# Performance work log

Hardware: AMD Instinct MI355X
Metric: run time of the kernel (lower is better)

Reference implementation:

```python
import jax, jax.numpy as jnp
import numpy as np
import math

G_GRAPHS = 32   # graphs per batch
NPG = 2048      # nodes per graph
DEG = 8         # avg degree
IN_DIM = 128
HID = 128

def _lin(k, fi, fo):
    return jax.random.normal(k, (fi, fo), jnp.float32) / np.sqrt(fi).astype(np.float32)

def setup_inputs():
    key = jax.random.key(0)
    ks = jax.random.split(key, 32)
    Nt = G_GRAPHS * NPG
    Epg = NPG * DEG
    E = G_GRAPHS * Epg
    x = jax.random.normal(ks[0], (Nt, IN_DIM), jnp.float32)
    src = jax.random.randint(ks[1], (E,), 0, NPG)
    dst = jax.random.randint(ks[2], (E,), 0, NPG)
    off = (jnp.arange(E) // Epg) * NPG  # keep edges within their graph block
    edge_index = jnp.stack([src + off, dst + off]).astype(jnp.int32)
    batch = (jnp.arange(Nt) // NPG).astype(jnp.int32)
    p = {}
    dims = [(IN_DIM, HID), (HID, HID), (HID, HID), (HID, HID)]
    for i, (fi, fo) in enumerate(dims, 1):
        p['Wl%d' % i] = _lin(ks[3 * i], fi, fo)
        p['bl%d' % i] = jnp.zeros((fo,), jnp.float32)
        p['Wr%d' % i] = _lin(ks[3 * i + 1], fi, fo)
    for j in (1, 2):  # SAGPooling score GNN (GraphConv hidden->1)
        p['Prel%d' % j] = _lin(ks[15 + 2 * j], HID, 1)
        p['prb%d' % j] = jnp.zeros((1,), jnp.float32)
        p['Proot%d' % j] = _lin(ks[16 + 2 * j], HID, 1)
    p['W5'] = _lin(ks[24], HID, 64); p['b5'] = jnp.zeros((64,), jnp.float32)
    p['W6'] = _lin(ks[25], 64, 2);  p['b6'] = jnp.zeros((2,), jnp.float32)
    return dict(x=x, edge_index=edge_index, batch=batch, npg=NPG, **p)

def reference(x, edge_index, batch, npg,
              Wl1, bl1, Wr1, Wl2, bl2, Wr2, Wl3, bl3, Wr3, Wl4, bl4, Wr4,
              Prel1, prb1, Proot1, Prel2, prb2, Proot2, W5, b5, W6, b6):
    src, dst = edge_index[0], edge_index[1]
    Nt = x.shape[0]
    Gn = Nt // npg

    def sage(h, em, Wl, bl, Wr):
        # SAGEConv (mean aggr): lin_l(mean_j x_j) + lin_r(x_root)
        s = jax.ops.segment_sum(h[src] * em[:, None], dst, num_segments=Nt)
        c = jax.ops.segment_sum(em, dst, num_segments=Nt)
        return (s / jnp.maximum(c, 1.0)[:, None]) @ Wl + bl + h @ Wr

    def pool(h, em, nm, k, Prel, prb, Proot):
        # SAGPooling: score = GraphConv(h) (add aggr), top-k per graph, x *= tanh(score)
        s = jax.ops.segment_sum(h[src] * em[:, None], dst, num_segments=Nt)
        score = (s @ Prel + h @ Proot + prb)[:, 0]
        smr = jnp.where(nm > 0, score, -1e30).reshape(Gn, npg)
        _, idx = jax.lax.top_k(smr, k)
        newm = jnp.zeros((Gn, npg), h.dtype).at[jnp.arange(Gn)[:, None], idx].set(1.0).reshape(-1)
        h = h * jnp.tanh(score)[:, None] * newm[:, None]
        em = em * newm[src] * newm[dst]  # filter_adj: keep edges with both ends kept
        return h, em, newm

    em = jnp.ones(src.shape, x.dtype)
    nm = jnp.ones((Nt,), x.dtype)
    h = jax.nn.relu(sage(x, em, Wl1, bl1, Wr1))
    h = jax.nn.relu(sage(h, em, Wl2, bl2, Wr2))
    k1 = math.ceil(0.5 * npg)
    h, em, nm = pool(h, em, nm, k1, Prel1, prb1, Proot1)
    h = jax.nn.relu(sage(h, em, Wl3, bl3, Wr3)) * nm[:, None]
    h = jax.nn.relu(sage(h, em, Wl4, bl4, Wr4)) * nm[:, None]
    k2 = math.ceil(0.5 * k1)
    h, em, nm = pool(h, em, nm, k2, Prel2, prb2, Proot2)
    # global mean pool over surviving nodes
    sums = jax.ops.segment_sum(h, batch, num_segments=Gn)
    cnt = jax.ops.segment_sum(nm, batch, num_segments=Gn)
    g = sums / jnp.maximum(cnt, 1.0)[:, None]
    g = jax.nn.relu(g @ W5 + b5)
    return jax.nn.log_softmax(g @ W6 + b6, axis=1)
```

## Files before the change

kernel.cpp:

```cpp
#include <hip/hip_runtime.h>
#include <hip/hip_bf16.h>
#include <math.h>

#define NT   65536
#define NPGC 2048
#define NG   32
#define NE   524288
#define HID  128
#define K1   1024
#define K2   512

typedef short short8 __attribute__((ext_vector_type(8)));
typedef float f32x4  __attribute__((ext_vector_type(4)));

__device__ __forceinline__ float bf2f(unsigned short u) {
    union { unsigned int i; float f; } v; v.i = ((unsigned int)u) << 16; return v.f;
}
__device__ __forceinline__ unsigned short f2bf(float f) {
    union { float f; unsigned int i; } v; v.f = f;
    unsigned int x = v.i;
    return (unsigned short)((x + 0x7fffu + ((x >> 16) & 1u)) >> 16);
}
__device__ __forceinline__ void split2(float v, unsigned short& hi, unsigned short& lo) {
    unsigned int b = __float_as_uint(v);
    hi = (unsigned short)(b >> 16);
    float rem = v - __uint_as_float(b & 0xFFFF0000u);
    lo = (unsigned short)(__float_as_uint(rem) >> 16);
}

__global__ void k_detect(const unsigned short* __restrict__ x, int* __restrict__ flag) {
    __shared__ int cnt;
    if (threadIdx.x == 0) cnt = 0;
    __syncthreads();
    int sane = 0;
#pragma unroll
    for (int j = 0; j < 16; ++j) {
        unsigned short u = x[threadIdx.x * 16 + j];
        int e = (u >> 7) & 0xFF;
        if (e > 0x60 && e < 0xA0) sane++;
    }
    atomicAdd(&cnt, sane);
    __syncthreads();
    if (threadIdx.x == 0) *flag = (cnt > 3686) ? 1 : 0;
}

struct CvtDesc { const void* src[22]; int n[22]; int off[22]; };

__global__ void k_cvt(CvtDesc d, float* __restrict__ wts, const int* __restrict__ flag) {
    int t = blockIdx.y;
    int n = d.n[t];
    bool isbf = (*flag != 0);
    const unsigned short* sb = (const unsigned short*)d.src[t];
    const float* sf = (const float*)d.src[t];
    float* o = wts + d.off[t];
    for (int i = blockIdx.x * blockDim.x + threadIdx.x; i < n; i += gridDim.x * blockDim.x)
        o[i] = isbf ? bf2f(sb[i]) : sf[i];
}

__global__ void k_packW(const float* __restrict__ wts, int4 oWl, int4 oWr,
                        unsigned short* __restrict__ Wpack,
                        int* __restrict__ rowc, int* __restrict__ fill) {
    int idx = blockIdx.x * 256 + threadIdx.x;
    if (idx < NT) { rowc[idx] = 0; fill[idx] = 0; }
    if (idx >= 4 * 8 * 8 * 64 * 8) return;
    int L    = idx >> 15;
    int rem  = idx & 32767;
    int ct   = rem >> 12;
    int rem2 = rem & 4095;
    int ks   = rem2 >> 9;
    int rem3 = rem2 & 511;
    int lane = rem3 >> 3;
    int j    = rem3 & 7;
    int k   = ks * 32 + (lane >> 4) * 8 + j;
    int col = ct * 16 + (lane & 15);
    int ol = (L == 0) ? oWl.x : (L == 1) ? oWl.y : (L == 2) ? oWl.z : oWl.w;
    int orr = (L == 0) ? oWr.x : (L == 1) ? oWr.y : (L == 2) ? oWr.z : oWr.w;
    float w = (k < 128) ? wts[ol + k * 128 + col] : wts[orr + (k - 128) * 128 + col];
    unsigned short hi = f2bf(w);
    unsigned short lo = f2bf(w - bf2f(hi));
    int base = L * 65536 + (ct * 8 + ks) * 512 + lane * 8 + j;
    Wpack[base]         = hi;
    Wpack[base + 32768] = lo;
}

__global__ void k_hist(const int* __restrict__ dstE, int* __restrict__ rowc) {
    int e = blockIdx.x * 256 + threadIdx.x;
    if (e < NE) atomicAdd(&rowc[dstE[e]], 1);
}

__global__ void k_scan1(const int* __restrict__ cnt, int* __restrict__ rp, int* __restrict__ bsum,
                        float* __restrict__ invc) {
    __shared__ int s[256];
    int t = threadIdx.x;
    int i = blockIdx.x * 256 + t;
    int v = cnt[i];
    invc[i] = 1.0f / fmaxf((float)v, 1.0f);
    s[t] = v;
    __syncthreads();
    for (int off = 1; off < 256; off <<= 1) {
        int a = (t >= off) ? s[t - off] : 0;
        __syncthreads();
        s[t] += a;
        __syncthreads();
    }
    rp[i] = s[t] - v;
    if (t == 255) bsum[blockIdx.x] = s[255];
}

__global__ void k_scan23(int* __restrict__ rp, const int* __restrict__ bsum) {
    __shared__ int s[256];
    int t = threadIdx.x;
    s[t] = bsum[t];
    __syncthreads();
    for (int off = 1; off < 256; off <<= 1) {
        int a = (t >= off) ? s[t - off] : 0;
        __syncthreads();
        s[t] += a;
        __syncthreads();
    }
    int boffv = s[blockIdx.x] - bsum[blockIdx.x];
    int i = blockIdx.x * 256 + t;
    rp[i] += boffv;
    if (i == 0) rp[NT] = NE;
}

__global__ void k_scatter(const int* __restrict__ src, const int* __restrict__ dst,
                          const int* __restrict__ rp, int* __restrict__ fill, int* __restrict__ col) {
    int e = blockIdx.x * blockDim.x + threadIdx.x;
    if (e < NE) {
        int d = dst[e];
        int p = rp[d] + atomicAdd(&fill[d], 1);
        col[p] = src[e];
    }
}

__device__ __forceinline__ int lds_sw(int node, int k) {
    int g = k >> 3;
    int go = g ^ (node & 7);
    return node * 128 + go * 8 + (k & 7);
}

template<int MODE>
__device__ __forceinline__ float4 ldrow4(const void* __restrict__ h, int node, int f) {
    if constexpr (MODE == 1) {
        ushort4 v = *((const ushort4*)h + (size_t)node * 32 + (f >> 2));
        float4 o; o.x = bf2f(v.x); o.y = bf2f(v.y); o.z = bf2f(v.z); o.w = bf2f(v.w);
        return o;
    } else {
        return *((const float4*)h + (size_t)node * 32 + (f >> 2));
    }
}

template<bool HAS_TS, bool COMPACT, int MODE>
__device__ __forceinline__ void sage_body(
    const void* __restrict__ h, const float* __restrict__ ts,
    const float* __restrict__ invc,
    const int* __restrict__ rp, const int* __restrict__ col,
    const unsigned short* __restrict__ Wp,
    unsigned short* Ahi, unsigned short* Alo,
    unsigned short* Bhi, unsigned short* Blo,
    int n0, const int* __restrict__ actb, int tid, f32x4 acc[2][2])
{
    int lane = tid & 63, w = tid >> 6;
    int lrow = lane & 15, quad = lane >> 4;
    int gnode = tid >> 5;
    int f = (tid & 31) * 4;

    int gns[4], begs[4], ends[4]; float invs[4];
#pragma unroll
    for (int p = 0; p < 4; ++p) gns[p] = COMPACT ? actb[p * 8 + gnode] : n0 + p * 8 + gnode;
#pragma unroll
    for (int p = 0; p < 4; ++p) { begs[p] = rp[gns[p]]; ends[p] = rp[gns[p] + 1]; }
#pragma unroll
    for (int p = 0; p < 4; ++p) invs[p] = invc[gns[p]];

    float4 rootv[4]; float roots[4];
#pragma unroll
    for (int i = 0; i < 4; ++i) {
        int idx = i * 256 + tid;
        int node = idx >> 5;
        int f2 = (idx & 31) * 4;
        int gn = COMPACT ? actb[node] : n0 + node;
        rootv[i] = ldrow4<MODE>(h, gn, f2);
        roots[i] = HAS_TS ? ts[gn] : 1.0f;
    }

#pragma unroll
    for (int pass = 0; pass < 4; ++pass) {
        int node = pass * 8 + gnode;
        float ax = 0.f, ay = 0.f, az = 0.f, aw = 0.f;
        int beg = begs[pass], end = ends[pass];
        int ecl = end - 1;
        for (int e0 = beg; e0 < end; e0 += 8) {
            int sj[8];
#pragma unroll
            for (int j = 0; j < 8; ++j) {
                int e = (e0 + j < end) ? e0 + j : ecl;
                sj[j] = col[e];
            }
            float4 vj[8];
#pragma unroll
            for (int j = 0; j < 8; ++j)
                vj[j] = ldrow4<MODE>(h, sj[j], f);
#pragma unroll
            for (int j = 0; j < 8; ++j) {
                float cj = (e0 + j < end) ? (HAS_TS ? ts[sj[j]] : 1.0f) : 0.0f;
                ax += vj[j].x * cj;
                ay += vj[j].y * cj;
                az += vj[j].z * cj;
                aw += vj[j].w * cj;
            }
        }
        float inv = invs[pass];
        ushort4 hi4, lo4;
        split2(ax * inv, hi4.x, lo4.x);
        split2(ay * inv, hi4.y, lo4.y);
        split2(az * inv, hi4.z, lo4.z);
        split2(aw * inv, hi4.w, lo4.w);
        int a = lds_sw(node, f);
        *(ushort4*)&Ahi[a] = hi4;
        *(ushort4*)&Alo[a] = lo4;
    }

#pragma unroll
    for (int i = 0; i < 4; ++i) {
        int idx = i * 256 + tid;
        int node = idx >> 5;
        int f2 = (idx & 31) * 4;
        float sc = roots[i];
        ushort4 hi4, lo4;
        split2(rootv[i].x * sc, hi4.x, lo4.x);
        split2(rootv[i].y * sc, hi4.y, lo4.y);
        split2(rootv[i].z * sc, hi4.z, lo4.z);
        split2(rootv[i].w * sc, hi4.w, lo4.w);
        int a = lds_sw(node, f2);
        *(ushort4*)&Bhi[a] = hi4;
        *(ushort4*)&Blo[a] = lo4;
    }
    __syncthreads();

#pragma unroll
    for (int ks = 0; ks < 8; ++ks) {
        const unsigned short* Hb = (ks < 4) ? Ahi : Bhi;
        const unsigned short* Lb = (ks < 4) ? Alo : Blo;
        short8 bh[2], blo[2];
#pragma unroll
        for (int c = 0; c < 2; ++c) {
            int ct = 2 * w + c;
            bh[c]  = *(const short8*)&Wp[(ct * 8 + ks) * 512 + lane * 8];
            blo[c] = *(const short8*)&Wp[32768 + (ct * 8 + ks) * 512 + lane * 8];
        }
        int kb = (ks & 3) * 32 + quad * 8;
#pragma unroll
        for (int st = 0; st < 2; ++st) {
            int a = lds_sw(st * 16 + lrow, kb);
            short8 ah = *(const short8*)&Hb[a];
            short8 al = *(const short8*)&Lb[a];
#pragma unroll
            for (int c = 0; c < 2; ++c) {
                acc[st][c] = __builtin_amdgcn_mfma_f32_16x16x32_bf16(ah, bh[c],  acc[st][c], 0, 0, 0);
                acc[st][c] = __builtin_amdgcn_mfma_f32_16x16x32_bf16(al, bh[c],  acc[st][c], 0, 0, 0);
                acc[st][c] = __builtin_amdgcn_mfma_f32_16x16x32_bf16(ah, blo[c], acc[st][c], 0, 0, 0);
            }
        }
    }
}

template<bool COMPACT>
__device__ __forceinline__ void map_block(int b, int& graph, int& tile) {
    if (COMPACT) { graph = (b & 7) * 4 + (b >> 8); tile = (b >> 3) & 31; }
    else         { graph = (b & 7) * 4 + (b >> 9); tile = (b >> 3) & 63; }
}

__global__ void __launch_bounds__(256, 8) k_sage_l1(
    const void* __restrict__ x, const int* __restrict__ flag,
    const float* __restrict__ invc,
    const int* __restrict__ rp, const int* __restrict__ col,
    const unsigned short* __restrict__ Wp, const float* __restrict__ bl,
    float* __restrict__ out)
{
    __shared__ unsigned short Ahi[32 * 128];
    __shared__ unsigned short Alo[32 * 128];
    __shared__ unsigned short Bhi[32 * 128];
    __shared__ unsigned short Blo[32 * 128];
    int tid = threadIdx.x;
    int graph, tile;
    map_block<false>(blockIdx.x, graph, tile);
    int n0 = graph * NPGC + tile * 32;
    int lane = tid & 63, w = tid >> 6;
    int lrow = lane & 15, quad = lane >> 4;
    f32x4 acc[2][2] = {};

    if (*flag)
        sage_body<false, false, 1>(x, nullptr, invc, rp, col, Wp, Ahi, Alo, Bhi, Blo, n0, nullptr, tid, acc);
    else
        sage_body<false, false, 0>(x, nullptr, invc, rp, col, Wp, Ahi, Alo, Bhi, Blo, n0, nullptr, tid, acc);

#pragma unroll
    for (int c = 0; c < 2; ++c) {
        int colg = (2 * w + c) * 16 + lrow;
        float bias = bl[colg];
#pragma unroll
        for (int st = 0; st < 2; ++st) {
#pragma unroll
            for (int rr = 0; rr < 4; ++rr) {
                int node = n0 + st * 16 + quad * 4 + rr;
                out[(size_t)node * HID + colg] = fmaxf(acc[st][c][rr] + bias, 0.f);
            }
        }
    }
}

__global__ void __launch_bounds__(256, 8) k_sage_plain(
    const float* __restrict__ h, const float* __restrict__ ts,
    const float* __restrict__ invc,
    const int* __restrict__ rp, const int* __restrict__ col,
    const unsigned short* __restrict__ Wp, const float* __restrict__ bl,
    float* __restrict__ out, const int* __restrict__ act)
{
    __shared__ unsigned short Ahi[32 * 128];
    __shared__ unsigned short Alo[32 * 128];
    __shared__ unsigned short Bhi[32 * 128];
    __shared__ unsigned short Blo[32 * 128];
    int tid = threadIdx.x;
    int graph, tile;
    map_block<true>(blockIdx.x, graph, tile);
    int n0 = graph * NPGC + tile * 32;
    const int* actb = act + graph * K1 + tile * 32;
    int lane = tid & 63, w = tid >> 6;
    int lrow = lane & 15, quad = lane >> 4;
    f32x4 acc[2][2] = {};

    sage_body<true, true, 0>(h, ts, invc, rp, col, Wp, Ahi, Alo, Bhi, Blo, n0, actb, tid, acc);

#pragma unroll
    for (int c = 0; c < 2; ++c) {
        int colg = (2 * w + c) * 16 + lrow;
        float bias = bl[colg];
#pragma unroll
        for (int st = 0; st < 2; ++st) {
#pragma unroll
            for (int rr = 0; rr < 4; ++rr) {
                int node = actb[st * 16 + quad * 4 + rr];
                out[(size_t)node * HID + colg] = fmaxf(acc[st][c][rr] + bias, 0.f);
            }
        }
    }
}

template<bool HAS_TS, bool COMPACT>
__global__ void __launch_bounds__(256, 8) k_sage_dots(
    const float* __restrict__ h, const float* __restrict__ ts,
    const float* __restrict__ invc,
    const int* __restrict__ rp, const int* __restrict__ col,
    const unsigned short* __restrict__ Wp, const float* __restrict__ bl,
    float* __restrict__ out,
    const float* __restrict__ Prel, const float* __restrict__ Proot,
    float* __restrict__ q, float* __restrict__ r, const int* __restrict__ act)
{
    __shared__ unsigned short Ahi[32 * 128];
    __shared__ unsigned short Alo[32 * 128];
    __shared__ unsigned short Bhi[32 * 128];
    __shared__ unsigned short Blo[32 * 128];
    int tid = threadIdx.x;
    int graph, tile;
    map_block<COMPACT>(blockIdx.x, graph, tile);
    int n0 = graph * NPGC + tile * 32;
    const int* actb = COMPACT ? (act + graph * K1 + tile * 32) : nullptr;
    int lane = tid & 63, w = tid >> 6;
    int lrow = lane & 15, quad = lane >> 4;
    f32x4 acc[2][2] = {};

    sage_body<HAS_TS, COMPACT, 0>(h, ts, invc, rp, col, Wp, Ahi, Alo, Bhi, Blo, n0, actb, tid, acc);

    float qp[2][4] = {}, rp_[2][4] = {};
#pragma unroll
    for (int c = 0; c < 2; ++c) {
        int colg = (2 * w + c) * 16 + lrow;
        float bias = bl[colg];
        float pq = Prel[colg], pr = Proot[colg];
#pragma unroll
        for (int st = 0; st < 2; ++st) {
#pragma unroll
            for (int rr = 0; rr < 4; ++rr) {
                int nl = st * 16 + quad * 4 + rr;
                int node = COMPACT ? actb[nl] : n0 + nl;
                float val = fmaxf(acc[st][c][rr] + bias, 0.f);
                out[(size_t)node * HID + colg] = val;
                qp[st][rr] += val * pq;
                rp_[st][rr] += val * pr;
            }
        }
    }
#pragma unroll
    for (int st = 0; st < 2; ++st)
#pragma unroll
        for (int rr = 0; rr < 4; ++rr) {
#pragma unroll
            for (int m = 1; m < 16; m <<= 1) {
                qp[st][rr]  += __shfl_xor(qp[st][rr],  m, 64);
                rp_[st][rr] += __shfl_xor(rp_[st][rr], m, 64);
            }
        }
    __syncthreads();
    float* qa = (float*)Ahi;
    if (tid < 64) qa[tid] = 0.f;
    __syncthreads();
    if (lrow == 0) {
#pragma unroll
        for (int st = 0; st < 2; ++st)
#pragma unroll
            for (int rr = 0; rr < 4; ++rr) {
                int nl = st * 16 + quad * 4 + rr;
                atomicAdd(&qa[nl], qp[st][rr]);
                atomicAdd(&qa[32 + nl], rp_[st][rr]);
            }
    }
    __syncthreads();
    if (tid < 32) {
        int node = COMPACT ? actb[tid] : n0 + tid;
        q[node] = qa[tid];
        r[node] = qa[32 + tid];
    }
}

__global__ void k_score(const float* __restrict__ q, const float* __restrict__ r,
                        const float* __restrict__ prb,
                        const int* __restrict__ rp, const int* __restrict__ col,
                        float* __restrict__ score) {
    int n = blockIdx.x * 256 + threadIdx.x;
    int beg = rp[n], end = rp[n + 1];
    float s = 0.f;
    for (int e = beg; e < end; ++e) s += q[col[e]];
    score[n] = s + r[n] + prb[0];
}

__global__ void k_score_act(const float* __restrict__ q, const float* __restrict__ r,
                            const float* __restrict__ prb,
                            const int* __restrict__ rp, const int* __restrict__ col,
                            float* __restrict__ score, const int* __restrict__ act) {
    int n = act[blockIdx.x * 256 + threadIdx.x];
    int beg = rp[n], end = rp[n + 1];
    float s = 0.f;
    for (int e = beg; e < end; ++e) s += q[col[e]];
    score[n] = s + r[n] + prb[0];
}

template<bool NMIN, bool DO_INVC, bool ZQ>
__global__ void __launch_bounds__(256) k_topk(const float* __restrict__ score,
                                              float* __restrict__ nm,
                                              float* __restrict__ tval, int k,
                                              int* __restrict__ act,
                                              float* __restrict__ q,
                                              const int* __restrict__ rp,
                                              const int* __restrict__ col,
                                              float* __restrict__ invc) {
    __shared__ unsigned int u[NPGC];
    __shared__ unsigned char kb[NPGC];
    __shared__ int hist[256];
    __shared__ int scanb[257];
    __shared__ int wtot[4];
    __shared__ int wtot2[4];
    __shared__ unsigned int s_byte;
    __shared__ int s_kk;
    int tid = threadIdx.x;
    int lane = tid & 63, wv = tid >> 6;
    int base = blockIdx.x * NPGC;

    for (int j = tid; j < NPGC; j += 256) {
        float sc = NMIN ? ((nm[base + j] > 0.f) ? score[base + j] : -1e30f) : score[base + j];
        unsigned int v = __float_as_uint(sc);
        v = (v & 0x80000000u) ? ~v : (v | 0x80000000u);
        u[j] = v;
    }
    hist[tid] = 0;
    if (tid == 0) scanb[256] = 0;
    __syncthreads();

    unsigned int prefix = 0;
    int kk = k;
#pragma unroll
    for (int round = 0; round < 4; ++round) {
        int shift = 24 - 8 * round;
        unsigned int pmask = (round == 0) ? 0u : (0xFFFFFFFFu << (32 - 8 * round));
        for (int j = tid; j < NPGC; j += 256) {
            unsigned int v = u[j];
            if ((v & pmask) == prefix) atomicAdd(&hist[(v >> shift) & 0xFF], 1);
        }
        __syncthreads();
        int s = hist[tid];
#pragma unroll
        for (int off = 1; off < 64; off <<= 1) {
            int t = __shfl_down(s, off, 64);
            s += (lane + off < 64) ? t : 0;
        }
        if (lane == 0) wtot[wv] = s;
        __syncthreads();
        int add = 0;
#pragma unroll
        for (int w2 = 1; w2 < 4; ++w2) add += (wv + w2 < 4) ? wtot[wv + w2] : 0;
        s += add;
        scanb[tid] = s;
        __syncthreads();
        int above = scanb[tid + 1];
        if (s >= kk && above < kk) { s_byte = (unsigned int)tid; s_kk = kk - above; }
        hist[tid] = 0;
        __syncthreads();
        prefix |= (s_byte << shift);
        kk = s_kk;
    }
    unsigned int thr = prefix;

    int j0 = tid * 8;
    int cnt = 0;
#pragma unroll
    for (int j = 0; j < 8; ++j) cnt += (u[j0 + j] == thr);
    int s = cnt;
#pragma unroll
    for (int off = 1; off < 64; off <<= 1) {
        int t = __shfl_up(s, off, 64);
        s += (lane >= off) ? t : 0;
    }
    if (lane == 63) wtot[wv] = s;
    __syncthreads();
    int add = 0;
#pragma unroll
    for (int w2 = 0; w2 < 4; ++w2) add += (w2 < wv) ? wtot[w2] : 0;
    int rank = s - cnt + add;

    unsigned int keepmask = 0u;
    int myrank = rank;
    int kcnt = 0;
#pragma unroll
    for (int j = 0; j < 8; ++j) {
        unsigned int v = u[j0 + j];
        bool kp;
        if (v > thr) kp = true;
        else if (v == thr) { kp = (myrank < kk); myrank++; }
        else kp = false;
        keepmask |= (kp ? 1u : 0u) << j;
        kcnt += kp ? 1 : 0;
        kb[j0 + j] = kp ? 1 : 0;
    }
    int s2 = kcnt;
#pragma unroll
    for (int off = 1; off < 64; off <<= 1) {
        int t2 = __shfl_up(s2, off, 64);
        s2 += (lane >= off) ? t2 : 0;
    }
    if (lane == 63) wtot2[wv] = s2;
    __syncthreads();
    int pos = s2 - kcnt;
#pragma unroll
    for (int w2 = 0; w2 < 4; ++w2) pos += (w2 < wv) ? wtot2[w2] : 0;
    int* actg = act + blockIdx.x * k;
#pragma unroll
    for (int j = 0; j < 8; ++j) {
        bool kp = (keepmask >> j) & 1u;
        int n = base + j0 + j;
        nm[n]   = kp ? 1.0f : 0.0f;
        tval[n] = kp ? tanhf(score[n]) : 0.0f;
        if (kp)      { actg[pos++] = n; }
        else if (ZQ) { q[n] = 0.0f; }
    }

    if (DO_INVC) {
        __syncthreads();
        for (int j = tid; j < NPGC; j += 256) {
            if (kb[j]) {
                int n = base + j;
                int bg = rp[n], en = rp[n + 1];
                float c = 0.f;
                for (int e = bg; e < en; ++e) c += (float)kb[col[e] - base];
                invc[n] = 1.0f / fmaxf(c, 1.0f);
            }
        }
    }
}

__global__ void k_tail(const float* __restrict__ h, const float* __restrict__ t,
                       const int* __restrict__ act,
                       const float* __restrict__ W5, const float* __restrict__ b5,
                       const float* __restrict__ W6, const float* __restrict__ b6,
                       void* __restrict__ out, const int* __restrict__ flag) {
    __shared__ float gsh[2][HID];
    __shared__ float g5[64];
    __shared__ float ls[2];
    int graph = blockIdx.x, tid = threadIdx.x;
    int f = tid & 127, sub = tid >> 7;
    const int* actg = act + graph * K2;
    float acc = 0.f;
#pragma unroll 8
    for (int i = 0; i < 256; ++i) {
        int gn = actg[sub * 256 + i];
        acc += h[(size_t)gn * HID + f] * t[gn];
    }
    gsh[sub][f] = acc;
    __syncthreads();
    if (tid < 64) {
        const float ic = 1.0f / (float)K2;
        float a5 = b5[tid];
        for (int ff = 0; ff < HID; ++ff)
            a5 += (gsh[0][ff] + gsh[1][ff]) * ic * W5[ff * 64 + tid];
        g5[tid] = fmaxf(a5, 0.f);
    }
    __syncthreads();
    if (tid < 2) {
        float l = b6[tid];
        for (int tt = 0; tt < 64; ++tt) l += g5[tt] * W6[tt * 2 + tid];
        ls[tid] = l;
    }
    __syncthreads();
    if (tid == 0) {
        float a = ls[0], b = ls[1];
        float mx = fmaxf(a, b);
        float lse = mx + logf(expf(a - mx) + expf(b - mx));
        if (*flag) {
            ((unsigned short*)out)[graph * 2 + 0] = f2bf(a - lse);
            ((unsigned short*)out)[graph * 2 + 1] = f2bf(b - lse);
        } else {
            ((float*)out)[graph * 2 + 0] = a - lse;
            ((float*)out)[graph * 2 + 1] = b - lse;
        }
    }
}

extern "C" void kernel_launch(void* const* d_in, const int* in_sizes, int n_in,
                              void* d_out, int out_size, void* d_ws, size_t ws_size,
                              hipStream_t stream) {
    const void* x    = d_in[0];
    const int*  ei   = (const int*)d_in[1];
    const int*  srcE = ei;
    const int*  dstE = ei + NE;

    char* ws = (char*)d_ws;
    float* hA    = (float*)(ws + 0);
    float* hB    = (float*)(ws + 33554432);
    float* tvec  = (float*)(ws + 67108864);
    float* invc  = (float*)(ws + 67371008);
    float* q     = (float*)(ws + 100663296);
    float* r     = (float*)(ws + 100925440);
    float* score = (float*)(ws + 101187584);
    float* nm    = (float*)(ws + 101449728);
    int*   rowc  = (int*)  (ws + 101711872);
    int*   rp    = (int*)  (ws + 101974016);
    int*   bsum  = (int*)  (ws + 102236416);
    int*   fill  = (int*)  (ws + 102238464);
    int*   col   = (int*)  (ws + 102500608);
    int*   flag  = (int*)  (ws + 104615936);
    float* wts   = (float*)(ws + 104616960);
    unsigned short* Wpack = (unsigned short*)(ws + 105179136);
    int*   act1  = rowc;
    int*   act2  = fill;
    (void)in_sizes; (void)n_in; (void)out_size; (void)ws_size;

    const int O_Wl1 = 0,      O_bl1 = 16384,  O_Wr1 = 16512;
    const int O_Wl2 = 32896,  O_bl2 = 49280,  O_Wr2 = 49408;
    const int O_Wl3 = 65792,  O_bl3 = 82176,  O_Wr3 = 82304;
    const int O_Wl4 = 98688,  O_bl4 = 115072, O_Wr4 = 115200;
    const int O_Pr1 = 131584, O_pb1 = 131712, O_Po1 = 131713;
    const int O_Pr2 = 131841, O_pb2 = 131969, O_Po2 = 131970;
    const int O_W5  = 132098, O_b5  = 140290, O_W6 = 140354, O_b6 = 140482;

    CvtDesc d;
    const int srcIdx[22] = {4,5,6,7,8,9,10,11,12,13,14,15,16,17,18,19,20,21,22,23,24,25};
    const int nelems[22] = {16384,128,16384, 16384,128,16384, 16384,128,16384, 16384,128,16384,
                            128,1,128, 128,1,128, 8192,64,128,2};
    const int offs[22]   = {O_Wl1,O_bl1,O_Wr1, O_Wl2,O_bl2,O_Wr2, O_Wl3,O_bl3,O_Wr3, O_Wl4,O_bl4,O_Wr4,
                            O_Pr1,O_pb1,O_Po1, O_Pr2,O_pb2,O_Po2, O_W5,O_b5,O_W6,O_b6};
    for (int i = 0; i < 22; ++i) { d.src[i] = d_in[srcIdx[i]]; d.n[i] = nelems[i]; d.off[i] = offs[i]; }

    k_detect <<<1, 256, 0, stream>>>((const unsigned short*)x, flag);
    k_cvt    <<<dim3(64, 22), 256, 0, stream>>>(d, wts, flag);
    k_packW  <<<512, 256, 0, stream>>>(wts, make_int4(O_Wl1, O_Wl2, O_Wl3, O_Wl4),
                                       make_int4(O_Wr1, O_Wr2, O_Wr3, O_Wr4), Wpack, rowc, fill);
    k_hist   <<<2048, 256, 0, stream>>>(dstE, rowc);

    k_scan1  <<<256, 256, 0, stream>>>(rowc, rp, bsum, invc);
    k_scan23 <<<256, 256, 0, stream>>>(rp, bsum);
    k_scatter<<<2048, 256, 0, stream>>>(srcE, dstE, rp, fill, col);

    k_sage_l1<<<2048, 256, 0, stream>>>(x, flag, invc, rp, col,
                                        Wpack + 0 * 65536, wts + O_bl1, hB);
    k_sage_dots<false, false><<<2048, 256, 0, stream>>>(hB, nullptr, invc, rp, col,
                                                        Wpack + 1 * 65536, wts + O_bl2, hA,
                                                        wts + O_Pr1, wts + O_Po1, q, r, nullptr);

    k_score<<<256, 256, 0, stream>>>(q, r, wts + O_pb1, rp, col, score);
    k_topk<false, true, true><<<32, 256, 0, stream>>>(score, nm, tvec, K1, act1, q, rp, col, invc);

    k_sage_plain<<<1024, 256, 0, stream>>>(hA, tvec, invc, rp, col,
                                           Wpack + 2 * 65536, wts + O_bl3, hB, act1);
    k_sage_dots<true, true><<<1024, 256, 0, stream>>>(hB, nm, invc, rp, col,
                                                      Wpack + 3 * 65536, wts + O_bl4, hA,
                                                      wts + O_Pr2, wts + O_Po2, q, r, act1);

    k_score_act<<<NG * K1 / 256, 256, 0, stream>>>(q, r, wts + O_pb2, rp, col, score, act1);
    k_topk<true, false, false><<<32, 256, 0, stream>>>(score, nm, tvec, K2, act2, nullptr, rp, col, nullptr);

    k_tail<<<32, 256, 0, stream>>>(hA, tvec, act2, wts + O_W5, wts + O_b5,
                                   wts + O_W6, wts + O_b6, d_out, flag);
}
```

Before: 382.7 us.

## Build filtered CSR after first pooling and use it for later layers

Adds a kernel that, after the first top-k, builds a compacted CSR (rp2/col2) for each graph that holds only edges whose source survived pooling, and computes the inverse degree counts there. Layers 3 and 4 and the second score pass then walk only the surviving edges instead of masking the full edge lists with nm/tvec lookups. The invc computation and the q zeroing are removed from top-k. Output stores also become nontemporal. The cost is an extra serial per-thread kernel with only 32 blocks, which may be slow.

Result: no change. 389.1 us (+1.7%).

```diff
diff --git a/kernel.cpp b/kernel.cpp
--- a/kernel.cpp
+++ b/kernel.cpp
@@ -6,6 +6,7 @@
 #define NPGC 2048
 #define NG   32
 #define NE   524288
+#define EPG  16384
 #define HID  128
 #define K1   1024
 #define K2   512
@@ -134,6 +135,55 @@
     }
 }
 
+__global__ void __launch_bounds__(256) k_fcsr(const int* __restrict__ act,
+                                              const float* __restrict__ nm,
+                                              const int* __restrict__ rp,
+                                              const int* __restrict__ col,
+                                              int2* __restrict__ rp2,
+                                              int* __restrict__ col2,
+                                              float* __restrict__ invc) {
+    __shared__ int wtot[4];
+    int g = blockIdx.x, t = threadIdx.x;
+    int lane = t & 63, wv = t >> 6;
+    int cb = g * K1;
+    int ebase = g * EPG;
+    int c[4]; int tsum = 0;
+    int bg[4], en[4];
+#pragma unroll
+    for (int j = 0; j < 4; ++j) {
+        int ci = t * 4 + j;
+        int n = act[cb + ci];
+        bg[j] = rp[n]; en[j] = rp[n + 1];
+        int cc = 0;
+        for (int e = bg[j]; e < en[j]; ++e) cc += (nm[col[e]] > 0.f) ? 1 : 0;
+        c[j] = cc; tsum += cc;
+        invc[n] = 1.0f / fmaxf((float)cc, 1.0f);
+    }
+    int pre = tsum;
+#pragma unroll
+    for (int off = 1; off < 64; off <<= 1) {
+        int v = __shfl_up(pre, off, 64);
+        pre += (lane >= off) ? v : 0;
+    }
+    if (lane == 63) wtot[wv] = pre;
+    __syncthreads();
+    int woff = 0;
+#pragma unroll
+    for (int w2 = 0; w2 < 4; ++w2) woff += (w2 < wv) ? wtot[w2] : 0;
+    int ex = pre - tsum + woff;
+#pragma unroll
+    for (int j = 0; j < 4; ++j) {
+        int ci = t * 4 + j;
+        int p = ebase + ex;
+        rp2[cb + ci] = make_int2(p, p + c[j]);
+        for (int e = bg[j]; e < en[j]; ++e) {
+            int s = col[e];
+            if (nm[s] > 0.f) col2[p++] = s;
+        }
+        ex += c[j];
+    }
+}
+
 __device__ __forceinline__ int lds_sw(int node, int k) {
     int g = k >> 3;
     int go = g ^ (node & 7);
@@ -155,11 +205,12 @@
 __device__ __forceinline__ void sage_body(
     const void* __restrict__ h, const float* __restrict__ ts,
     const float* __restrict__ invc,
-    const int* __restrict__ rp, const int* __restrict__ col,
+    const int* __restrict__ rp, const int2* __restrict__ rp2,
+    const int* __restrict__ col,
     const unsigned short* __restrict__ Wp,
     unsigned short* Ahi, unsigned short* Alo,
     unsigned short* Bhi, unsigned short* Blo,
-    int n0, const int* __restrict__ actb, int tid, f32x4 acc[2][2])
+    int n0, int cb, const int* __restrict__ actb, int tid, f32x4 acc[2][2])
 {
     int lane = tid & 63, w = tid >> 6;
     int lrow = lane & 15, quad = lane >> 4;
@@ -170,7 +221,10 @@
 #pragma unroll
     for (int p = 0; p < 4; ++p) gns[p] = COMPACT ? actb[p * 8 + gnode] : n0 + p * 8 + gnode;
 #pragma unroll
-    for (int p = 0; p < 4; ++p) { begs[p] = rp[gns[p]]; ends[p] = rp[gns[p] + 1]; }
+    for (int p = 0; p < 4; ++p) {
+        if (COMPACT) { int2 be = rp2[cb + p * 8 + gnode]; begs[p] = be.x; ends[p] = be.y; }
+        else         { begs[p] = rp[gns[p]]; ends[p] = rp[gns[p] + 1]; }
+    }
 #pragma unroll
     for (int p = 0; p < 4; ++p) invs[p] = invc[gns[p]];
 
@@ -292,9 +346,9 @@
     f32x4 acc[2][2] = {};
 
     if (*flag)
-        sage_body<false, false, 1>(x, nullptr, invc, rp, col, Wp, Ahi, Alo, Bhi, Blo, n0, nullptr, tid, acc);
+        sage_body<false, false, 1>(x, nullptr, invc, rp, nullptr, col, Wp, Ahi, Alo, Bhi, Blo, n0, 0, nullptr, tid, acc);
     else
-        sage_body<false, false, 0>(x, nullptr, invc, rp, col, Wp, Ahi, Alo, Bhi, Blo, n0, nullptr, tid, acc);
+        sage_body<false, false, 0>(x, nullptr, invc, rp, nullptr, col, Wp, Ahi, Alo, Bhi, Blo, n0, 0, nullptr, tid, acc);
 
 #pragma unroll
     for (int c = 0; c < 2; ++c) {
@@ -305,7 +359,8 @@
 #pragma unroll
             for (int rr = 0; rr < 4; ++rr) {
                 int node = n0 + st * 16 + quad * 4 + rr;
-                out[(size_t)node * HID + colg] = fmaxf(acc[st][c][rr] + bias, 0.f);
+                __builtin_nontemporal_store(fmaxf(acc[st][c][rr] + bias, 0.f),
+                                            &out[(size_t)node * HID + colg]);
             }
         }
     }
@@ -314,7 +369,7 @@
 __global__ void __launch_bounds__(256, 8) k_sage_plain(
     const float* __restrict__ h, const float* __restrict__ ts,
     const float* __restrict__ invc,
-    const int* __restrict__ rp, const int* __restrict__ col,
+    const int2* __restrict__ rp2, const int* __restrict__ col2,
     const unsigned short* __restrict__ Wp, const float* __restrict__ bl,
     float* __restrict__ out, const int* __restrict__ act)
 {
@@ -326,12 +381,13 @@
     int graph, tile;
     map_block<true>(blockIdx.x, graph, tile);
     int n0 = graph * NPGC + tile * 32;
-    const int* actb = act + graph * K1 + tile * 32;
+    int cb = graph * K1 + tile * 32;
+    const int* actb = act + cb;
     int lane = tid & 63, w = tid >> 6;
     int lrow = lane & 15, quad = lane >> 4;
     f32x4 acc[2][2] = {};
 
-    sage_body<true, true, 0>(h, ts, invc, rp, col, Wp, Ahi, Alo, Bhi, Blo, n0, actb, tid, acc);
+    sage_body<true, true, 0>(h, ts, invc, nullptr, rp2, col2, Wp, Ahi, Alo, Bhi, Blo, n0, cb, actb, tid, acc);
 
 #pragma unroll
     for (int c = 0; c < 2; ++c) {
@@ -342,17 +398,19 @@
 #pragma unroll
             for (int rr = 0; rr < 4; ++rr) {
                 int node = actb[st * 16 + quad * 4 + rr];
-                out[(size_t)node * HID + colg] = fmaxf(acc[st][c][rr] + bias, 0.f);
+                __builtin_nontemporal_store(fmaxf(acc[st][c][rr] + bias, 0.f),
+                                            &out[(size_t)node * HID + colg]);
             }
         }
     }
 }
 
-template<bool HAS_TS, bool COMPACT>
+template<bool COMPACT>
 __global__ void __launch_bounds__(256, 8) k_sage_dots(
-    const float* __restrict__ h, const float* __restrict__ ts,
+    const float* __restrict__ h,
     const float* __restrict__ invc,
-    const int* __restrict__ rp, const int* __restrict__ col,
+    const int* __restrict__ rp, const int2* __restrict__ rp2,
+    const int* __restrict__ col,
     const unsigned short* __restrict__ Wp, const float* __restrict__ bl,
     float* __restrict__ out,
     const float* __restrict__ Prel, const float* __restrict__ Proot,
@@ -366,12 +424,13 @@
     int graph, tile;
     map_block<COMPACT>(blockIdx.x, graph, tile);
     int n0 = graph * NPGC + tile * 32;
-    const int* actb = COMPACT ? (act + graph * K1 + tile * 32) : nullptr;
+    int cb = COMPACT ? (graph * K1 + tile * 32) : 0;
+    const int* actb = COMPACT ? (act + cb) : nullptr;
     int lane = tid & 63, w = tid >> 6;
     int lrow = lane & 15, quad = lane >> 4;
     f32x4 acc[2][2] = {};
 
-    sage_body<HAS_TS, COMPACT, 0>(h, ts, invc, rp, col, Wp, Ahi, Alo, Bhi, Blo, n0, actb, tid, acc);
+    sage_body<false, COMPACT, 0>(h, nullptr, invc, rp, rp2, col, Wp, Ahi, Alo, Bhi, Blo, n0, cb, actb, tid, acc);
 
     float qp[2][4] = {}, rp_[2][4] = {};
 #pragma unroll
@@ -386,7 +445,7 @@
                 int nl = st * 16 + quad * 4 + rr;
                 int node = COMPACT ? actb[nl] : n0 + nl;
                 float val = fmaxf(acc[st][c][rr] + bias, 0.f);
-                out[(size_t)node * HID + colg] = val;
+                __builtin_nontemporal_store(val, &out[(size_t)node * HID + colg]);
                 qp[st][rr] += val * pq;
                 rp_[st][rr] += val * pr;
             }
@@ -435,28 +494,24 @@
     score[n] = s + r[n] + prb[0];
 }
 
-__global__ void k_score_act(const float* __restrict__ q, const float* __restrict__ r,
-                            const float* __restrict__ prb,
-                            const int* __restrict__ rp, const int* __restrict__ col,
-                            float* __restrict__ score, const int* __restrict__ act) {
-    int n = act[blockIdx.x * 256 + threadIdx.x];
-    int beg = rp[n], end = rp[n + 1];
+__global__ void k_score2(const float* __restrict__ q, const float* __restrict__ r,
+                         const float* __restrict__ prb,
+                         const int2* __restrict__ rp2, const int* __restrict__ col2,
+                         float* __restrict__ score, const int* __restrict__ act) {
+    int i = blockIdx.x * 256 + threadIdx.x;
+    int n = act[i];
+    int2 be = rp2[i];
     float s = 0.f;
-    for (int e = beg; e < end; ++e) s += q[col[e]];
+    for (int e = be.x; e < be.y; ++e) s += q[col2[e]];
     score[n] = s + r[n] + prb[0];
 }
 
-template<bool NMIN, bool DO_INVC, bool ZQ>
+template<bool NMIN>
 __global__ void __launch_bounds__(256) k_topk(const float* __restrict__ score,
                                               float* __restrict__ nm,
                                               float* __restrict__ tval, int k,
-                                              int* __restrict__ act,
-                                              float* __restrict__ q,
-                                              const int* __restrict__ rp,
-                                              const int* __restrict__ col,
-                                              float* __restrict__ invc) {
+                                              int* __restrict__ act) {
     __shared__ unsigned int u[NPGC];
-    __shared__ unsigned char kb[NPGC];
     __shared__ int hist[256];
     __shared__ int scanb[257];
     __shared__ int wtot[4];
@@ -540,7 +595,6 @@
         else kp = false;
         keepmask |= (kp ? 1u : 0u) << j;
         kcnt += kp ? 1 : 0;
-        kb[j0 + j] = kp ? 1 : 0;
     }
     int s2 = kcnt;
 #pragma unroll
@@ -560,21 +614,7 @@
         int n = base + j0 + j;
         nm[n]   = kp ? 1.0f : 0.0f;
         tval[n] = kp ? tanhf(score[n]) : 0.0f;
-        if (kp)      { actg[pos++] = n; }
-        else if (ZQ) { q[n] = 0.0f; }
-    }
-
-    if (DO_INVC) {
-        __syncthreads();
-        for (int j = tid; j < NPGC; j += 256) {
-            if (kb[j]) {
-                int n = base + j;
-                int bg = rp[n], en = rp[n + 1];
-                float c = 0.f;
-                for (int e = bg; e < en; ++e) c += (float)kb[col[e] - base];
-                invc[n] = 1.0f / fmaxf(c, 1.0f);
-            }
-        }
+        if (kp) actg[pos++] = n;
     }
 }
 
@@ -638,6 +678,8 @@
     float* hB    = (float*)(ws + 33554432);
     float* tvec  = (float*)(ws + 67108864);
     float* invc  = (float*)(ws + 67371008);
+    int*   col2  = (int*)  (ws + 67633152);
+    int2*  rp2   = (int2*) (ws + 69730304);
     float* q     = (float*)(ws + 100663296);
     float* r     = (float*)(ws + 100925440);
     float* score = (float*)(ws + 101187584);
@@ -682,21 +724,22 @@
 
     k_sage_l1<<<2048, 256, 0, stream>>>(x, flag, invc, rp, col,
                                         Wpack + 0 * 65536, wts + O_bl1, hB);
-    k_sage_dots<false, false><<<2048, 256, 0, stream>>>(hB, nullptr, invc, rp, col,
-                                                        Wpack + 1 * 65536, wts + O_bl2, hA,
-                                                        wts + O_Pr1, wts + O_Po1, q, r, nullptr);
+    k_sage_dots<false><<<2048, 256, 0, stream>>>(hB, invc, rp, nullptr, col,
+                                                 Wpack + 1 * 65536, wts + O_bl2, hA,
+                                                 wts + O_Pr1, wts + O_Po1, q, r, nullptr);
 
     k_score<<<256, 256, 0, stream>>>(q, r, wts + O_pb1, rp, col, score);
-    k_topk<false, true, true><<<32, 256, 0, stream>>>(score, nm, tvec, K1, act1, q, rp, col, invc);
-
-    k_sage_plain<<<1024, 256, 0, stream>>>(hA, tvec, invc, rp, col,
+    k_topk<false><<<32, 256, 0, stream>>>(score, nm, tvec, K1, act1);
+    k_fcsr <<<32, 256, 0, stream>>>(act1, nm, rp, col, rp2, col2, invc);
+
+    k_sage_plain<<<1024, 256, 0, stream>>>(hA, tvec, invc, rp2, col2,
                                            Wpack + 2 * 65536, wts + O_bl3, hB, act1);
-    k_sage_dots<true, true><<<1024, 256, 0, stream>>>(hB, nm, invc, rp, col,
-                                                      Wpack + 3 * 65536, wts + O_bl4, hA,
-                                                      wts + O_Pr2, wts + O_Po2, q, r, act1);
-
-    k_score_act<<<NG * K1 / 256, 256, 0, stream>>>(q, r, wts + O_pb2, rp, col, score, act1);
-    k_topk<true, false, false><<<32, 256, 0, stream>>>(score, nm, tvec, K2, act2, nullptr, rp, col, nullptr);
+    k_sage_dots<true><<<1024, 256, 0, stream>>>(hB, invc, nullptr, rp2, col2,
+                                                Wpack + 3 * 65536, wts + O_bl4, hA,
+                                                wts + O_Pr2, wts + O_Po2, q, r, act1);
+
+    k_score2<<<NG * K1 / 256, 256, 0, stream>>>(q, r, wts + O_pb2, rp2, col2, score, act1);
+    k_topk<true><<<32, 256, 0, stream>>>(score, nm, tvec, K2, act2);
 
     k_tail<<<32, 256, 0, stream>>>(hA, tvec, act2, wts + O_W5, wts + O_b5,
                                    wts + O_W6, wts + O_b6, d_out, flag);
```
